# Kernel tuning notes

Hardware: AMD Instinct MI355X
Metric: run time of the kernel (lower is better)

The kernel has to match this reference:

```python
import jax, jax.numpy as jnp
from jax import lax
import numpy as np

B, H, W_, C, F = 4, 32, 32, 16, 16
KH, KW = 3, 3
L = 1.0


def setup_inputs() -> dict:
    key = jax.random.key(0)
    k1, k2, k3, k4 = jax.random.split(key, 4)
    inputs = jax.random.normal(k1, (B, H, W_, C), dtype=jnp.float32)
    # lecun_normal-style scales (stddev = 1/sqrt(fan_in))
    m_scale = 1.0 / np.sqrt(H * W_ * 1)
    g_scale = 1.0 / np.sqrt(KH * KW * C)
    M = jax.random.normal(k2, (H, W_, 1, H, W_, 1), dtype=jnp.float32) * m_scale
    Wp = jax.random.normal(k3, (H, W_, 1, H, W_, 1), dtype=jnp.float32) * m_scale
    G = jax.random.normal(k4, (H, W_, KH, KW, C, F), dtype=jnp.float32) * g_scale
    return {"inputs": inputs, "M": M, "Wp": Wp, "G": G}


def reference(inputs, M, Wp, G):
    b, h, w, c = inputs.shape
    kh, kw, f = G.shape[2], G.shape[3], G.shape[5]
    M2 = M[:, :, 0, :, :, 0]   # (i,j,p,q)
    W2 = Wp[:, :, 0, :, :, 0]  # (i,j,p,q)
    # first_term[b,i,j,c] = sum_pq M[i,j,p,q] * inputs[b,p,q,c]
    first = jnp.einsum('ijpq,bpqc->bijc', M2, inputs)
    # One big conv: kernel (kh,kw,c, h*w*f) gives shifted for every output pixel (i,j)
    K = jnp.transpose(G, (2, 3, 4, 0, 1, 5)).reshape(kh, kw, c, h * w * f)
    shifted = lax.conv_general_dilated(
        inputs, K, window_strides=(1, 1), padding='SAME',
        dimension_numbers=('NHWC', 'HWIO', 'NHWC'))
    shifted = shifted.reshape(b, h, w, h, w, f)  # (b,p,q,i,j,f)
    diff = jax.nn.relu(inputs[:, :, :, None, None, :] - shifted)  # (b,p,q,i,j,c)
    # second_term[b,i,j,c] = sum_pq W[i,j,p,q] * relu(inputs - shifted)[b,p,q,i,j,c]
    second = jnp.einsum('ijpq,bpqijc->bijc', W2, diff)
    return first - L * second
```

## Files before the change

### kernel.cpp

```cpp
#include <hip/hip_runtime.h>


typedef __attribute__((ext_vector_type(8))) short bf16x8;
typedef __attribute__((ext_vector_type(4))) float f32x4;

__device__ inline unsigned short f2bf(float x) {
    unsigned u = __float_as_uint(x);
    u += 0x7FFFu + ((u >> 16) & 1u);
    return (unsigned short)(u >> 16);
}
__device__ inline unsigned pack2(float a, float b) {
    return (unsigned)f2bf(a) | ((unsigned)f2bf(b) << 16);
}

__device__ inline void gld_lds16(const void* g, void* l) {
    __builtin_amdgcn_global_load_lds((const __attribute__((address_space(1))) void*)g,
                                     (__attribute__((address_space(3))) void*)l, 16, 0, 0);
}

__global__ __launch_bounds__(256) void build_pre(const float* __restrict__ inp,
                                                 const float* __restrict__ G,
                                                 uint4* __restrict__ A,
                                                 float4* __restrict__ Xf,
                                                 uint4* __restrict__ Gf,
                                                 float4* __restrict__ outz) {
    const int tid = blockIdx.x * 256 + threadIdx.x;
    const int u = tid >> 12;
    if (u >= 28) {
        const int gidx = tid - 114688;
        const int ijkk = gidx >> 6, l = gidx & 63;
        const int ij = ijkk / 5, kk = ijkk - ij * 5;
        const int quad = l >> 4, col = l & 15;
        const float* Gg = G + ij * 2304;
        float v[8];
#pragma unroll
        for (int j = 0; j < 8; ++j) {
            const int k = kk * 32 + quad * 8 + j;
            v[j] = (k < 144) ? Gg[k * 16 + col] : 0.f;
        }
        uint4 o;
        o.x = pack2(v[0], v[1]); o.y = pack2(v[2], v[3]);
        o.z = pack2(v[4], v[5]); o.w = pack2(v[6], v[7]);
        Gf[ij * 320 + kk * 64 + l] = o;
        return;
    }
    if (u >= 24) {
        outz[tid - 98304] = (float4){0.f, 0.f, 0.f, 0.f};
        return;
    }
    if (u >= 20) {
        const int idx = tid - 81920;
        const int tile = idx >> 6, ll = idx & 63;
        const int rowb = tile * 16 + (ll >> 4) * 4;
        const int col = ll & 15;
        float4 v;
        v.x = inp[(rowb + 0) * 16 + col];
        v.y = inp[(rowb + 1) * 16 + col];
        v.z = inp[(rowb + 2) * 16 + col];
        v.w = inp[(rowb + 3) * 16 + col];
        Xf[idx] = v;
        return;
    }
    const int row = tid & 4095;
    const int tile = row >> 4, m = row & 15;
    if (u >= 18) {
        const uint4 z = {0, 0, 0, 0};
        A[(tile * 5 + 4) * 64 + (u - 16) * 16 + m] = z;
        return;
    }
    const int tap = u >> 1, h = u & 1;
    const int dh = tap / 3, dw = tap - dh * 3;
    const int b = row >> 10, pq = row & 1023;
    const int p = pq >> 5, q = pq & 31;
    const int pp = p + dh - 1, qq = q + dw - 1;
    const int kk = tap >> 1, quad = (tap & 1) * 2 + h;
    uint4 o = {0, 0, 0, 0};
    if (((unsigned)pp < 32u) && ((unsigned)qq < 32u)) {
        const float4* s = (const float4*)(inp + b * 16384 + (pp * 32 + qq) * 16 + 8 * h);
        const float4 f0 = s[0], f1 = s[1];
        o.x = pack2(f0.x, f0.y); o.y = pack2(f0.z, f0.w);
        o.z = pack2(f1.x, f1.y); o.w = pack2(f1.z, f1.w);
    }
    A[(tile * 5 + kk) * 64 + quad * 16 + m] = o;
}

__global__ __launch_bounds__(512, 1) void inrf_main(
    const float* __restrict__ M,
    const float* __restrict__ Wp,
    const uint4* __restrict__ Gf,
    const uint4* __restrict__ Aw,
    const float4* __restrict__ Xf,
    float* __restrict__ out)
{
    const int bid = blockIdx.x;
    const int ijblk = bid & 31;
    const int tgrp  = bid >> 5;
    const int tile0 = tgrp * 32;
    const int bb    = tgrp >> 1;

    const int t = threadIdx.x, l = t & 63, w = t >> 6;
    const int quad = l >> 4;

    __shared__ __align__(16) uint4  Ab[2][4][5][64];
    __shared__ __align__(16) float4 Xb[2][4][64];

    auto stage = [&](int buf, int ct0) {
#pragma unroll
        for (int r = 0; r < 3; ++r) {
            const int s = w * 3 + r;
            if (s < 20) {
                const int ct = s / 5, kk = s - ct * 5;
                gld_lds16(&Aw[((ct0 + ct) * 5 + kk) * 64 + l], &Ab[buf][ct][kk][0]);
            } else {
                const int ct = s - 20;
                gld_lds16(&Xf[(ct0 + ct) * 64 + l], &Xb[buf][ct][0]);
            }
        }
    };

    stage(0, tile0);

    const int ij0 = ijblk * 32 + w * 4;
    bf16x8 Bf[4][5];
#pragma unroll
    for (int ij = 0; ij < 4; ++ij)
#pragma unroll
        for (int kk = 0; kk < 5; ++kk)
            Bf[ij][kk] = __builtin_bit_cast(bf16x8, Gf[(ij0 + ij) * 320 + kk * 64 + l]);

    float4 mwW[2][4], mwM[2][4];
    auto mwload = [&](int pbuf, int tgn) {
        const int pqb = (tgn & 63) * 16 + quad * 4;
#pragma unroll
        for (int jj = 0; jj < 4; ++jj) {
            mwW[pbuf][jj] = *(const float4*)&Wp[(ij0 + jj) * 1024 + pqb];
            mwM[pbuf][jj] = *(const float4*)&M [(ij0 + jj) * 1024 + pqb];
        }
    };

    mwload(0, tile0);

    float accv[4] = {0.f, 0.f, 0.f, 0.f};

    asm volatile("s_waitcnt vmcnt(0)" ::: "memory");
    __syncthreads();

    int buf = 0;
#pragma unroll 1
    for (int ph = 0; ph < 8; ++ph) {
        if (ph < 7) stage(buf ^ 1, tile0 + (ph + 1) * 4);
#pragma unroll
        for (int ct = 0; ct < 4; ++ct) {
            const int ctg = ph * 4 + ct;
            mwload((ct + 1) & 1, tile0 + ((ctg + 1) & 31));

            uint4 Af[5];
#pragma unroll
            for (int kk = 0; kk < 5; ++kk) Af[kk] = Ab[buf][ct][kk][l];
            const float4 vr = Xb[buf][ct][l];

            f32x4 C[4];
#pragma unroll
            for (int jj = 0; jj < 4; ++jj) C[jj] = (f32x4){0.f, 0.f, 0.f, 0.f};
#pragma unroll
            for (int kk = 0; kk < 5; ++kk) {
                const bf16x8 a = __builtin_bit_cast(bf16x8, Af[kk]);
#pragma unroll
                for (int jj = 0; jj < 4; ++jj)
                    C[jj] = __builtin_amdgcn_mfma_f32_16x16x32_bf16(
                                a, Bf[jj][kk], C[jj], 0, 0, 0);
            }

#pragma unroll
            for (int jj = 0; jj < 4; ++jj) {
                const float4 w2 = mwW[ct & 1][jj];
                const float4 m2 = mwM[ct & 1][jj];
                float a0 = accv[jj];
                a0 += m2.x * vr.x - w2.x * fmaxf(vr.x - C[jj][0], 0.f);
                a0 += m2.y * vr.y - w2.y * fmaxf(vr.y - C[jj][1], 0.f);
                a0 += m2.z * vr.z - w2.z * fmaxf(vr.z - C[jj][2], 0.f);
                a0 += m2.w * vr.w - w2.w * fmaxf(vr.w - C[jj][3], 0.f);
                accv[jj] = a0;
            }
        }
        asm volatile("s_waitcnt vmcnt(0)" ::: "memory");
        __syncthreads();
        buf ^= 1;
    }

#pragma unroll
    for (int jj = 0; jj < 4; ++jj) {
        float v = accv[jj];
        v += __shfl_xor(v, 16);
        v += __shfl_xor(v, 32);
        if (l < 16) atomicAdd(&out[bb * 16384 + (ij0 + jj) * 16 + l], v);
    }
}

extern "C" void kernel_launch(void* const* d_in, const int* in_sizes, int n_in,
                              void* d_out, int out_size, void* d_ws, size_t ws_size,
                              hipStream_t stream) {
    const float* inp = (const float*)d_in[0];
    const float* M   = (const float*)d_in[1];
    const float* Wp  = (const float*)d_in[2];
    const float* G   = (const float*)d_in[3];
    float* out = (float*)d_out;

    uint4*  A  = (uint4*)d_ws;
    float4* Xf = (float4*)((char*)d_ws + 1310720);
    uint4*  Gf = (uint4*)((char*)d_ws + 1572864);

    build_pre<<<dim3(1728), dim3(256), 0, stream>>>(inp, G, A, Xf, Gf, (float4*)out);
    inrf_main<<<dim3(256), dim3(512), 0, stream>>>(M, Wp, Gf, A, Xf, out);
}
```

Measured before the change: 102.2 us.

## Stage M and Wp tiles into LDS with triple-buffered async pipeline

M and Wp coefficients were read straight from global memory into registers each tile. They are now loaded into LDS through async global-to-LDS copies alongside the A and X tiles. The double buffer becomes a triple buffer with staged vmcnt waits, so prefetches can run two phases ahead. This aims to hide global load latency and cut register pressure, at the cost of more LDS and delicate manual vmcnt accounting.

```diff
diff --git a/kernel.cpp b/kernel.cpp
--- a/kernel.cpp
+++ b/kernel.cpp
@@ -101,25 +101,35 @@
     const int t = threadIdx.x, l = t & 63, w = t >> 6;
     const int quad = l >> 4;
 
-    __shared__ __align__(16) uint4  Ab[2][4][5][64];
-    __shared__ __align__(16) float4 Xb[2][4][64];
-
-    auto stage = [&](int buf, int ct0) {
-#pragma unroll
-        for (int r = 0; r < 3; ++r) {
-            const int s = w * 3 + r;
+    __shared__ __align__(16) uint4  Ab[3][4][5][64];
+    __shared__ __align__(16) float4 Xb[3][4][64];
+    __shared__ __align__(16) float  Mb[3][4][32][16];
+    __shared__ __align__(16) float  Wb[3][4][32][16];
+
+    auto stage = [&](int buf, int t0) {
+#pragma unroll
+        for (int r = 0; r < 5; ++r) {
+            const int s = w * 5 + r;
             if (s < 20) {
                 const int ct = s / 5, kk = s - ct * 5;
-                gld_lds16(&Aw[((ct0 + ct) * 5 + kk) * 64 + l], &Ab[buf][ct][kk][0]);
+                gld_lds16(&Aw[((t0 + ct) * 5 + kk) * 64 + l], &Ab[buf][ct][kk][0]);
+            } else if (s < 24) {
+                const int ct = s - 20;
+                gld_lds16(&Xf[(t0 + ct) * 64 + l], &Xb[buf][ct][0]);
+            } else if (s < 32) {
+                const int q = s - 24, ct = q >> 1, h = q & 1;
+                const int ijg = ijblk * 32 + h * 16 + (l >> 2);
+                const int pq0 = ((t0 + ct) & 63) * 16 + (l & 3) * 4;
+                gld_lds16(&M[ijg * 1024 + pq0], &Mb[buf][ct][h * 16][0]);
             } else {
-                const int ct = s - 20;
-                gld_lds16(&Xf[(ct0 + ct) * 64 + l], &Xb[buf][ct][0]);
+                const int q = s - 32, ct = q >> 1, h = q & 1;
+                const int ijg = ijblk * 32 + h * 16 + (l >> 2);
+                const int pq0 = ((t0 + ct) & 63) * 16 + (l & 3) * 4;
+                gld_lds16(&Wp[ijg * 1024 + pq0], &Wb[buf][ct][h * 16][0]);
             }
         }
     };
 
-    stage(0, tile0);
-
     const int ij0 = ijblk * 32 + w * 4;
     bf16x8 Bf[4][5];
 #pragma unroll
@@ -128,32 +138,22 @@
         for (int kk = 0; kk < 5; ++kk)
             Bf[ij][kk] = __builtin_bit_cast(bf16x8, Gf[(ij0 + ij) * 320 + kk * 64 + l]);
 
-    float4 mwW[2][4], mwM[2][4];
-    auto mwload = [&](int pbuf, int tgn) {
-        const int pqb = (tgn & 63) * 16 + quad * 4;
-#pragma unroll
-        for (int jj = 0; jj < 4; ++jj) {
-            mwW[pbuf][jj] = *(const float4*)&Wp[(ij0 + jj) * 1024 + pqb];
-            mwM[pbuf][jj] = *(const float4*)&M [(ij0 + jj) * 1024 + pqb];
-        }
-    };
-
-    mwload(0, tile0);
+    stage(0, tile0);
+    stage(1, tile0 + 4);
+    stage(2, tile0 + 8);
 
     float accv[4] = {0.f, 0.f, 0.f, 0.f};
 
-    asm volatile("s_waitcnt vmcnt(0)" ::: "memory");
-    __syncthreads();
-
-    int buf = 0;
 #pragma unroll 1
     for (int ph = 0; ph < 8; ++ph) {
-        if (ph < 7) stage(buf ^ 1, tile0 + (ph + 1) * 4);
+        if (ph < 6)      asm volatile("s_waitcnt vmcnt(10)" ::: "memory");
+        else if (ph == 6) asm volatile("s_waitcnt vmcnt(5)" ::: "memory");
+        else              asm volatile("s_waitcnt vmcnt(0)" ::: "memory");
+        __builtin_amdgcn_s_barrier();
+
+        const int buf = ph % 3;
 #pragma unroll
         for (int ct = 0; ct < 4; ++ct) {
-            const int ctg = ph * 4 + ct;
-            mwload((ct + 1) & 1, tile0 + ((ctg + 1) & 31));
-
             uint4 Af[5];
 #pragma unroll
             for (int kk = 0; kk < 5; ++kk) Af[kk] = Ab[buf][ct][kk][l];
@@ -173,8 +173,8 @@
 
 #pragma unroll
             for (int jj = 0; jj < 4; ++jj) {
-                const float4 w2 = mwW[ct & 1][jj];
-                const float4 m2 = mwM[ct & 1][jj];
+                const float4 w2 = *(const float4*)&Wb[buf][ct][w * 4 + jj][quad * 4];
+                const float4 m2 = *(const float4*)&Mb[buf][ct][w * 4 + jj][quad * 4];
                 float a0 = accv[jj];
                 a0 += m2.x * vr.x - w2.x * fmaxf(vr.x - C[jj][0], 0.f);
                 a0 += m2.y * vr.y - w2.y * fmaxf(vr.y - C[jj][1], 0.f);
@@ -183,9 +183,9 @@
                 accv[jj] = a0;
             }
         }
-        asm volatile("s_waitcnt vmcnt(0)" ::: "memory");
-        __syncthreads();
-        buf ^= 1;
+
+        __builtin_amdgcn_s_barrier();
+        if (ph < 5) stage(buf, tile0 + (ph + 3) * 4);
     }
 
 #pragma unroll
```

Measured after the change: 148.6 us. 45.4% more time.
